# Optimization experiments

Measured on AMD Instinct MI355X. Metric: run time of the kernel, lower is better.

Reference implementation:

```python
import jax, jax.numpy as jnp
import numpy as np
from jax import lax

B, C, H, W = 8192, 256, 5, 5
G = 8
SE_HID = 64        # max(8, 256 // 4)
GN_EPS = 1e-5
MM_EPS = 1e-8


def group_norm(x, gamma, beta):
    # x: [B, C, H, W]; normalize per (group, H, W)
    b = x.shape[0]
    xg = x.reshape(b, G, C // G, H, W)
    mean = xg.mean(axis=(2, 3, 4), keepdims=True)
    var = xg.var(axis=(2, 3, 4), keepdims=True)
    xg = (xg - mean) * lax.rsqrt(var + GN_EPS)
    xn = xg.reshape(b, C, H, W)
    return xn * gamma[None, :, None, None] + beta[None, :, None, None]


def setup_inputs() -> dict:
    key = jax.random.key(0)
    ks = jax.random.split(key, 10)
    x = jax.random.normal(ks[0], (B, C, H, W), dtype=jnp.float32)
    pair_mask = (jax.random.uniform(ks[1], (B, 1, H, W)) < 0.8).astype(jnp.float32)
    s1 = 1.0 / np.sqrt(C)
    W1 = jax.random.normal(ks[2], (C, C), dtype=jnp.float32) * s1          # 1x1 conv
    W2 = jax.random.normal(ks[3], (C, C, 3, 3), dtype=jnp.float32) * (s1 / 3.0)
    g1 = jnp.ones((C,), jnp.float32); b1 = jnp.zeros((C,), jnp.float32)
    g2 = jnp.ones((C,), jnp.float32); b2 = jnp.zeros((C,), jnp.float32)
    fc1_w = jax.random.normal(ks[4], (SE_HID, C), dtype=jnp.float32) * s1
    fc1_b = jnp.zeros((SE_HID,), jnp.float32)
    fc2_w = jax.random.normal(ks[5], (C, SE_HID), dtype=jnp.float32) / np.sqrt(SE_HID)
    fc2_b = jnp.zeros((C,), jnp.float32)
    return {"x": x, "pair_mask": pair_mask, "W1": W1, "g1": g1, "b1": b1,
            "W2": W2, "g2": g2, "b2": b2,
            "fc1_w": fc1_w, "fc1_b": fc1_b, "fc2_w": fc2_w, "fc2_b": fc2_b}


def reference(x, pair_mask, W1, g1, b1, W2, g2, b2, fc1_w, fc1_b, fc2_w, fc2_b):
    residual = x
    # conv1: 1x1, no bias -> channel mixing
    out = jnp.einsum('bchw,oc->bohw', x, W1)
    out = jax.nn.gelu(group_norm(out, g1, b1), approximate=False)
    # conv2: 3x3, padding=1, no bias
    out = lax.conv_general_dilated(out, W2, window_strides=(1, 1),
                                   padding=((1, 1), (1, 1)),
                                   dimension_numbers=('NCHW', 'OIHW', 'NCHW'))
    out = jax.nn.gelu(group_norm(out, g2, b2), approximate=False)
    out = out + residual
    # masked SE
    denom = jnp.maximum(pair_mask.sum(axis=(-1, -2)), MM_EPS)   # [B,1]
    pooled = (out * pair_mask).sum(axis=(-1, -2)) / denom       # [B,C]
    h = jax.nn.gelu(pooled @ fc1_w.T + fc1_b, approximate=False)
    gate = jax.nn.sigmoid(h @ fc2_w.T + fc2_b)                  # [B,C]
    out = out * gate[:, :, None, None] * pair_mask              # SE mask
    out = out * pair_mask                                       # final mask
    return out, gate
```

## Files before the change

kernel.cpp:

```cpp
#include <hip/hip_runtime.h>
#include <math.h>


typedef short v8s  __attribute__((ext_vector_type(8)));
typedef short v4s  __attribute__((ext_vector_type(4)));
typedef float v16f __attribute__((ext_vector_type(16)));
typedef float v4f  __attribute__((ext_vector_type(4)));

#define NTHREADS 512
#define NB 2
#define CPB 560
#define YROWS 49
#define YSB (YROWS*CPB)

#define Y_BYTES  (NB*YSB)
#define GB_OFF   (Y_BYTES)
#define MASK_OFF (GB_OFF + 4096)
#define POOL_OFF (MASK_OFF + 256)
#define H_OFF    (POOL_OFF + 2048)
#define GATE_OFF (H_OFF + 512)
#define INVD_OFF (GATE_OFF + 2048)
#define SMEM_BYTES (INVD_OFF + 64)

__device__ __forceinline__ unsigned short f2bf(float f){
  unsigned u = __float_as_uint(f);
  u = u + 0x7fffu + ((u >> 16) & 1u);
  return (unsigned short)(u >> 16);
}
__device__ __forceinline__ float gelu_f(float v){
  float z  = fabsf(v) * 0.70710678118654752f;
  float t  = __builtin_amdgcn_rcpf(fmaf(0.3275911f, z, 1.0f));
  float e  = __builtin_amdgcn_exp2f(-z*z*1.4426950408889634f);
  float p  = fmaf(1.061405429f, t, -1.453152027f);
  p = fmaf(p, t, 1.421413741f);
  p = fmaf(p, t, -0.284496736f);
  p = fmaf(p, t, 0.254829592f);
  float er = fmaf(-p*t, e, 1.0f);
  er = __builtin_copysignf(er, v);
  return 0.5f*v*(1.0f + er);
}

__device__ __forceinline__ void v16store(char* dst, const v16f &v){
  #pragma unroll
  for (int q=0;q<4;++q){
    v4f t; t[0]=v[4*q]; t[1]=v[4*q+1]; t[2]=v[4*q+2]; t[3]=v[4*q+3];
    *(v4f*)(dst + q*1024) = t;
  }
}
__device__ __forceinline__ void v16addload(const char* src, v16f &v){
  #pragma unroll
  for (int q=0;q<4;++q){
    v4f t = *(const v4f*)(src + q*1024);
    v[4*q]+=t[0]; v[4*q+1]+=t[1]; v[4*q+2]+=t[2]; v[4*q+3]+=t[3];
  }
}

__global__ void prep_kernel(const float* __restrict__ W1, const float* __restrict__ W2,
                            const float* __restrict__ fc1w, const float* __restrict__ fc2w,
                            unsigned short* __restrict__ w1p, unsigned short* __restrict__ w2p,
                            float* __restrict__ fc1t, float* __restrict__ fc2t)
{
  int t = blockIdx.x*blockDim.x + threadIdx.x;
  int stride = gridDim.x*blockDim.x;
  for (int i=t; i<16*256*16; i+=stride){
    int s=i>>12, o=(i>>4)&255, kk=i&15;
    w1p[i] = f2bf(W1[o*256 + s*16 + kk]);
  }
  for (int i=t; i<144*256*16; i+=stride){
    int s=i>>12, o=(i>>4)&255, kk=i&15;
    int kh = (s >= 72) ? 1 : 0;
    int r  = s - kh*72;
    int tap = r>>3, u = r&7;
    int ck = kh*128 + u*16 + kk;
    w2p[i] = f2bf(W2[o*2304 + ck*9 + tap]);
  }
  for (int i=t; i<256*64; i+=stride){ int c=i>>6, h=i&63; fc1t[i]=fc1w[h*256+c]; }
  for (int i=t; i<64*256; i+=stride){ int k=i>>8, c=i&255; fc2t[i]=fc2w[c*64+k]; }
}

__global__ __launch_bounds__(NTHREADS, 4) void lrb_main(
    const float* __restrict__ xg, const float* __restrict__ maskg,
    const float* __restrict__ g1, const float* __restrict__ b1,
    const float* __restrict__ g2, const float* __restrict__ b2,
    const unsigned short* __restrict__ w1p, const unsigned short* __restrict__ w2p,
    const float* __restrict__ fc1t, const float* __restrict__ fc1b,
    const float* __restrict__ fc2t, const float* __restrict__ fc2b,
    float* __restrict__ outg, float* __restrict__ gateg)
{
  extern __shared__ char smem[];
  float* OUTF = (float*)smem;
  float* GB   = (float*)(smem + GB_OFF);
  float* MS   = (float*)(smem + MASK_OFF);
  float* POOL = (float*)(smem + POOL_OFF);
  float* HS   = (float*)(smem + H_OFF);
  float* GT   = (float*)(smem + GATE_OFF);
  float* INVD = (float*)(smem + INVD_OFF);

  const int tid  = threadIdx.x;
  const int lane = tid & 63;
  const int wid  = tid >> 6;
  const int mp   = wid >> 1;
  const int kh   = wid & 1;
  const int p    = lane & 31;
  const int half = lane >> 5;
  const int hx   = half << 4;
  const bool pv  = (p < 25);
  const int b0   = blockIdx.x * NB;

  {
    int4 z4; z4.x=z4.y=z4.z=z4.w=0;
    for (int i = tid; i < NB*24*35; i += NTHREADS){
      int nbb = i / 840;
      int rem = i - nbb*840;
      int rr  = 25 + rem/35, cc = rem - (rem/35)*35;
      *(int4*)(smem + nbb*YSB + rr*CPB + cc*16) = z4;
    }
    if (tid < 256){
      GB[tid]=g1[tid]; GB[256+tid]=b1[tid]; GB[512+tid]=g2[tid]; GB[768+tid]=b2[tid];
    }
    if (tid >= 256 && tid < 256 + NB*32){
      int t2 = tid - 256;
      int nbb = t2>>5, pp = t2&31;
      MS[t2] = (pp < 25) ? maskg[(size_t)(b0+nbb)*25 + pp] : 0.f;
    }
  }

  const int pr = p/5, ps = p - 5*(p/5);
  const int pbase = pv ? (7*pr + ps) : 0;
  const int bcol  = hx + kh*256;
  const char* w1c = (const char*)w1p;
  const char* w2c = (const char*)w2p;
  const int aoff1 = (wid*32 + p)*32 + hx;
  const char* w2k = w2c + kh*589824 + mp*2048 + p*32 + hx;
  const char* Yb1[2] = { smem + p*CPB + hx, smem + YSB + p*CPB + hx };

  v8s A1[3], B1[3][2];
  #pragma unroll
  for (int s0=0; s0<3; ++s0) A1[s0] = *(const v8s*)(w1c + s0*8192 + aoff1);

  for (int i = tid; i < NB*25*32; i += NTHREADS){
    int nbb = i / 800;
    int rem = i - nbb*800;
    int pp  = rem >> 5;
    int c8  = rem & 31;
    const float* src = xg + ((size_t)(b0+nbb)*256 + c8*8)*25 + pp;
    v8s pk;
    #pragma unroll
    for (int k=0;k<8;++k) pk[k] = (short)f2bf(src[k*25]);
    *(v8s*)(smem + nbb*YSB + pp*CPB + c8*16) = pk;
  }
  __syncthreads();

  if (tid < NB){
    float s=0.f;
    #pragma unroll
    for (int pp=0;pp<25;++pp) s += MS[tid*32+pp];
    INVD[tid] = __builtin_amdgcn_rcpf(fmaxf(s, 1e-8f));
  }

  v16f acc1_0, acc1_1;
  #pragma unroll
  for (int j=0;j<16;++j){ acc1_0[j]=0.f; acc1_1[j]=0.f; }
  #pragma unroll
  for (int s0=0; s0<3; ++s0){
    B1[s0][0] = *(const v8s*)(Yb1[0] + s0*32);
    B1[s0][1] = *(const v8s*)(Yb1[1] + s0*32);
  }
  #pragma unroll
  for (int s=0; s<16; ++s){
    __builtin_amdgcn_s_setprio(1);
    acc1_0 = __builtin_amdgcn_mfma_f32_32x32x16_bf16(A1[s%3], B1[s%3][0], acc1_0, 0,0,0);
    acc1_1 = __builtin_amdgcn_mfma_f32_32x32x16_bf16(A1[s%3], B1[s%3][1], acc1_1, 0,0,0);
    __builtin_amdgcn_s_setprio(0);
    if (s+3 < 16){
      A1[s%3] = *(const v8s*)(w1c + (s+3)*8192 + aoff1);
      B1[s%3][0] = *(const v8s*)(Yb1[0] + (s+3)*32);
      B1[s%3][1] = *(const v8s*)(Yb1[1] + (s+3)*32);
    }
  }

  {
    float s0a=0.f,q0a=0.f,s1a=0.f,q1a=0.f;
    #pragma unroll
    for (int j=0;j<16;++j){
      float v0 = acc1_0[j], v1 = acc1_1[j];
      s0a+=v0; q0a+=v0*v0; s1a+=v1; q1a+=v1*v1;
    }
    #pragma unroll
    for (int off=1; off<64; off<<=1){
      s0a += __shfl_xor(s0a, off, 64); q0a += __shfl_xor(q0a, off, 64);
      s1a += __shfl_xor(s1a, off, 64); q1a += __shfl_xor(q1a, off, 64);
    }
    __syncthreads();

    const int grow = pbase + 8;
    float mu0 = s0a*(1.f/800.f), mu1 = s1a*(1.f/800.f);
    float rstd0 = rsqrtf(q0a*(1.f/800.f) - mu0*mu0 + 1e-5f);
    float rstd1 = rsqrtf(q1a*(1.f/800.f) - mu1*mu1 + 1e-5f);
    if (pv){
      #pragma unroll
      for (int nt=0; nt<2; ++nt){
        float mu = nt ? mu1 : mu0, rstd = nt ? rstd1 : rstd0;
        char* dst = smem + nt*YSB + grow*CPB + wid*64 + half*8;
        #pragma unroll
        for (int q=0;q<4;++q){
          v4s pk;
          #pragma unroll
          for (int i2=0;i2<4;++i2){
            int ch = wid*32 + q*8 + half*4 + i2;
            float v = nt ? acc1_1[4*q+i2] : acc1_0[4*q+i2];
            float f = (v-mu)*rstd*GB[ch]+GB[256+ch];
            pk[i2] = (short)f2bf(gelu_f(f));
          }
          *(v4s*)(dst + q*16) = pk;
        }
      }
    }
  }
  {
    int4 z4; z4.x=z4.y=z4.z=z4.w=0;
    for (int i = tid; i < NB*12*35; i += NTHREADS){
      int nbb = i / 420;
      int rem = i - nbb*420;
      int rr  = rem/35, cc = rem - (rem/35)*35;
      int row = rr < 8 ? rr : (rr < 10 ? rr + 5 : rr + 10);
      *(int4*)(smem + nbb*YSB + row*CPB + cc*16) = z4;
    }
  }

  v8s A2[3][2], B2[3][2];
  #pragma unroll
  for (int s0=0; s0<3; ++s0){
    A2[s0][0] = *(const v8s*)(w2k + s0*8192);
    A2[s0][1] = *(const v8s*)(w2k + s0*8192 + 1024);
  }
  __syncthreads();

  v16f acc2_00, acc2_01, acc2_10, acc2_11;
  #pragma unroll
  for (int j=0;j<16;++j){ acc2_00[j]=0.f; acc2_01[j]=0.f; acc2_10[j]=0.f; acc2_11[j]=0.f; }

  {
    int bq = pv ? pbase*CPB : 41*CPB;
    const int bd = pv ? 7*CPB : 0;
    int tb = 0;

    #pragma unroll
    for (int s0=0; s0<3; ++s0){
      B2[s0][0] = *(const v8s*)(smem + bq + bcol + s0*32);
      B2[s0][1] = *(const v8s*)(smem + YSB + bq + bcol + s0*32);
    }

#define C2_STEP(S, PF) do { \
    __builtin_amdgcn_s_setprio(1); \
    acc2_00 = __builtin_amdgcn_mfma_f32_32x32x16_bf16(A2[(S)%3][0], B2[(S)%3][0], acc2_00, 0,0,0); \
    acc2_01 = __builtin_amdgcn_mfma_f32_32x32x16_bf16(A2[(S)%3][0], B2[(S)%3][1], acc2_01, 0,0,0); \
    acc2_10 = __builtin_amdgcn_mfma_f32_32x32x16_bf16(A2[(S)%3][1], B2[(S)%3][0], acc2_10, 0,0,0); \
    acc2_11 = __builtin_amdgcn_mfma_f32_32x32x16_bf16(A2[(S)%3][1], B2[(S)%3][1], acc2_11, 0,0,0); \
    __builtin_amdgcn_s_setprio(0); \
    if (PF) { \
      const char* ap_ = w2k + tb + ((S)+3)*8192; \
      A2[(S)%3][0] = *(const v8s*)(ap_); \
      A2[(S)%3][1] = *(const v8s*)(ap_ + 1024); \
      const int ro_ = (((S)+3) < 24) ? (((S)+3)>>3)*CPB : 7*CPB; \
      const int co_ = (((S)+3)&7)*32; \
      B2[(S)%3][0] = *(const v8s*)(smem + bq + ro_ + bcol + co_); \
      B2[(S)%3][1] = *(const v8s*)(smem + YSB + bq + ro_ + bcol + co_); \
    } \
  } while(0)

    #pragma unroll 1
    for (int tr=0; tr<2; ++tr){
      #pragma unroll
      for (int s=0; s<24; ++s) C2_STEP(s, 1);
      tb += 196608;
      bq += bd;
    }
    #pragma unroll
    for (int s=0; s<21; ++s) C2_STEP(s, 1);
    #pragma unroll
    for (int s=21; s<24; ++s) C2_STEP(s, 0);
#undef C2_STEP
  }
  __syncthreads();

  {
    char* EXw = smem + (kh^1)*16384 + mp*4096 + (lane<<4);
    const char* EXr = smem + kh*16384 + mp*4096 + (lane<<4);
    if (kh==0) v16store(EXw, acc2_01); else v16store(EXw, acc2_00);
    __syncthreads();
    if (kh==0) v16addload(EXr, acc2_00); else v16addload(EXr, acc2_01);
    __syncthreads();
    if (kh==0) v16store(EXw, acc2_11); else v16store(EXw, acc2_10);
    __syncthreads();
    if (kh==0) v16addload(EXr, acc2_10); else v16addload(EXr, acc2_11);
  }
  v16f F0 = (kh==0) ? acc2_00 : acc2_01;
  v16f F1 = (kh==0) ? acc2_10 : acc2_11;

  {
    float s0a=0.f,q0a=0.f,s1a=0.f,q1a=0.f;
    #pragma unroll
    for (int j=0;j<16;++j){
      float v0=F0[j], v1=F1[j];
      s0a+=v0; q0a+=v0*v0; s1a+=v1; q1a+=v1*v1;
    }
    #pragma unroll
    for (int off=1; off<64; off<<=1){
      s0a += __shfl_xor(s0a, off, 64); q0a += __shfl_xor(q0a, off, 64);
      s1a += __shfl_xor(s1a, off, 64); q1a += __shfl_xor(q1a, off, 64);
    }
    __syncthreads();

    float mu0 = s0a*(1.f/800.f), mu1 = s1a*(1.f/800.f);
    float rstd0 = rsqrtf(q0a*(1.f/800.f) - mu0*mu0 + 1e-5f);
    float rstd1 = rsqrtf(q1a*(1.f/800.f) - mu1*mu1 + 1e-5f);
    const float* xr = xg + ((size_t)(b0+kh)*256 + mp*64)*25 + p;
    if (pv){
      #pragma unroll
      for (int j=0;j<16;++j){
        int crow = (j&3) + 8*(j>>2) + 4*half;
        {
          int ch = mp*64 + crow;
          float f = (F0[j]-mu0)*rstd0*GB[512+ch]+GB[768+ch];
          f = gelu_f(f) + xr[crow*25];
          OUTF[kh*6400 + ch*25 + p] = f;
        }
        {
          int ch = mp*64 + 32 + crow;
          float f = (F1[j]-mu1)*rstd1*GB[512+ch]+GB[768+ch];
          f = gelu_f(f) + xr[(32+crow)*25];
          OUTF[kh*6400 + ch*25 + p] = f;
        }
      }
    }
  }
  __syncthreads();

  {
    int nbb = tid >> 8, ch = tid & 255;
    const float* of = OUTF + nbb*6400 + ch*25;
    const float* ms = MS + nbb*32;
    float dot = 0.f;
    #pragma unroll
    for (int pp=0; pp<25; ++pp) dot = fmaf(of[pp], ms[pp], dot);
    POOL[nbb*256 + ch] = dot;
  }
  __syncthreads();

  {
    int nbb  = tid >> 8;
    int hid  = (tid >> 2) & 63;
    int part = tid & 3;
    const float* pl = POOL + nbb*256 + part*64;
    const float* wp = fc1t + part*64*64 + hid;
    float dot = 0.f;
    #pragma unroll 8
    for (int c=0;c<64;++c) dot += wp[c*64]*pl[c];
    dot += __shfl_xor(dot, 1, 64);
    dot += __shfl_xor(dot, 2, 64);
    if (part == 0)
      HS[nbb*64+hid] = gelu_f(fmaf(INVD[nbb], dot, fc1b[hid]));
  }
  __syncthreads();
  {
    int ch = tid & 255, nbb = tid >> 8;
    const float* hp = HS + nbb*64;
    float dot = 0.f;
    #pragma unroll 8
    for (int k=0;k<64;++k) dot += fc2t[k*256+ch]*hp[k];
    dot += fc2b[ch];
    float gv = __builtin_amdgcn_rcpf(1.0f + __builtin_amdgcn_exp2f(-dot*1.4426950408889634f));
    GT[nbb*256+ch] = gv;
    gateg[(size_t)(b0+nbb)*256+ch] = gv;
  }
  __syncthreads();

  for (int i = tid; i < NB*1600; i += NTHREADS){
    int nbb = i / 1600;
    int r4  = i - nbb*1600;
    int e0  = r4*4;
    v4f o4 = *(const v4f*)(OUTF + nbb*6400 + e0);
    #pragma unroll
    for (int k=0;k<4;++k){
      int e = e0+k;
      int ch = e/25;
      int pp = e - ch*25;
      o4[k] = o4[k] * GT[nbb*256+ch] * MS[nbb*32+pp];
    }
    *(v4f*)(outg + (size_t)(b0+nbb)*6400 + e0) = o4;
  }
}

extern "C" void kernel_launch(void* const* d_in, const int* in_sizes, int n_in,
                              void* d_out, int out_size, void* d_ws, size_t ws_size,
                              hipStream_t stream)
{
  const float* xg   = (const float*)d_in[0];
  const float* pm   = (const float*)d_in[1];
  const float* W1   = (const float*)d_in[2];
  const float* g1   = (const float*)d_in[3];
  const float* b1   = (const float*)d_in[4];
  const float* W2   = (const float*)d_in[5];
  const float* g2   = (const float*)d_in[6];
  const float* b2   = (const float*)d_in[7];
  const float* fc1w = (const float*)d_in[8];
  const float* fc1b = (const float*)d_in[9];
  const float* fc2w = (const float*)d_in[10];
  const float* fc2b = (const float*)d_in[11];

  float* outg  = (float*)d_out;
  float* gateg = outg + (size_t)8192*256*25;

  unsigned short* w1p = (unsigned short*)d_ws;
  unsigned short* w2p = w1p + 16*256*16;
  float* fc1t = (float*)(w2p + 144*256*16);
  float* fc2t = fc1t + 256*64;

  prep_kernel<<<dim3(512), dim3(256), 0, stream>>>(W1, W2, fc1w, fc2w, w1p, w2p, fc1t, fc2t);

  hipFuncSetAttribute(reinterpret_cast<const void*>(lrb_main),
                      hipFuncAttributeMaxDynamicSharedMemorySize, (int)SMEM_BYTES);
  lrb_main<<<dim3(4096), dim3(NTHREADS), SMEM_BYTES, stream>>>(
      xg, pm, g1, b1, g2, b2, w1p, w2p, fc1t, fc1b, fc2t, fc2b, outg, gateg);
}
```

Measured before the change: 540.6 us.

## Restructure 3x3 conv as per-wave 144-step MFMA loop with bf16 staging for occupancy

```diff
diff --git a/kernel.cpp b/kernel.cpp
--- a/kernel.cpp
+++ b/kernel.cpp
@@ -9,8 +9,8 @@
 
 #define NTHREADS 512
 #define NB 2
-#define CPB 560
-#define YROWS 49
+#define CPB 528
+#define YROWS 26
 #define YSB (YROWS*CPB)
 
 #define Y_BYTES  (NB*YSB)
@@ -26,6 +26,9 @@
   unsigned u = __float_as_uint(f);
   u = u + 0x7fffu + ((u >> 16) & 1u);
   return (unsigned short)(u >> 16);
+}
+__device__ __forceinline__ float bf2f(unsigned short u){
+  return __uint_as_float(((unsigned)u) << 16);
 }
 __device__ __forceinline__ float gelu_f(float v){
   float z  = fabsf(v) * 0.70710678118654752f;
@@ -40,21 +43,6 @@
   return 0.5f*v*(1.0f + er);
 }
 
-__device__ __forceinline__ void v16store(char* dst, const v16f &v){
-  #pragma unroll
-  for (int q=0;q<4;++q){
-    v4f t; t[0]=v[4*q]; t[1]=v[4*q+1]; t[2]=v[4*q+2]; t[3]=v[4*q+3];
-    *(v4f*)(dst + q*1024) = t;
-  }
-}
-__device__ __forceinline__ void v16addload(const char* src, v16f &v){
-  #pragma unroll
-  for (int q=0;q<4;++q){
-    v4f t = *(const v4f*)(src + q*1024);
-    v[4*q]+=t[0]; v[4*q+1]+=t[1]; v[4*q+2]+=t[2]; v[4*q+3]+=t[3];
-  }
-}
-
 __global__ void prep_kernel(const float* __restrict__ W1, const float* __restrict__ W2,
                             const float* __restrict__ fc1w, const float* __restrict__ fc2w,
                             unsigned short* __restrict__ w1p, unsigned short* __restrict__ w2p,
@@ -68,17 +56,14 @@
   }
   for (int i=t; i<144*256*16; i+=stride){
     int s=i>>12, o=(i>>4)&255, kk=i&15;
-    int kh = (s >= 72) ? 1 : 0;
-    int r  = s - kh*72;
-    int tap = r>>3, u = r&7;
-    int ck = kh*128 + u*16 + kk;
-    w2p[i] = f2bf(W2[o*2304 + ck*9 + tap]);
+    int tap=s>>4, u=s&15;
+    w2p[i] = f2bf(W2[o*2304 + (u*16+kk)*9 + tap]);
   }
   for (int i=t; i<256*64; i+=stride){ int c=i>>6, h=i&63; fc1t[i]=fc1w[h*256+c]; }
   for (int i=t; i<64*256; i+=stride){ int k=i>>8, c=i&255; fc2t[i]=fc2w[c*64+k]; }
 }
 
-__global__ __launch_bounds__(NTHREADS, 4) void lrb_main(
+__global__ __launch_bounds__(NTHREADS, 6) void lrb_main(
     const float* __restrict__ xg, const float* __restrict__ maskg,
     const float* __restrict__ g1, const float* __restrict__ b1,
     const float* __restrict__ g2, const float* __restrict__ b2,
@@ -88,7 +73,7 @@
     float* __restrict__ outg, float* __restrict__ gateg)
 {
   extern __shared__ char smem[];
-  float* OUTF = (float*)smem;
+  unsigned short* OUTFu = (unsigned short*)smem;
   float* GB   = (float*)(smem + GB_OFF);
   float* MS   = (float*)(smem + MASK_OFF);
   float* POOL = (float*)(smem + POOL_OFF);
@@ -99,8 +84,6 @@
   const int tid  = threadIdx.x;
   const int lane = tid & 63;
   const int wid  = tid >> 6;
-  const int mp   = wid >> 1;
-  const int kh   = wid & 1;
   const int p    = lane & 31;
   const int half = lane >> 5;
   const int hx   = half << 4;
@@ -109,34 +92,40 @@
 
   {
     int4 z4; z4.x=z4.y=z4.z=z4.w=0;
-    for (int i = tid; i < NB*24*35; i += NTHREADS){
-      int nbb = i / 840;
-      int rem = i - nbb*840;
-      int rr  = 25 + rem/35, cc = rem - (rem/35)*35;
-      *(int4*)(smem + nbb*YSB + rr*CPB + cc*16) = z4;
-    }
-    if (tid < 256){
-      GB[tid]=g1[tid]; GB[256+tid]=b1[tid]; GB[512+tid]=g2[tid]; GB[768+tid]=b2[tid];
-    }
-    if (tid >= 256 && tid < 256 + NB*32){
-      int t2 = tid - 256;
+    if (tid < 2*33){
+      int nt = tid/33, cc = tid - nt*33;
+      *(int4*)(smem + nt*YSB + 25*CPB + cc*16) = z4;
+    }
+    if (tid >= 64 && tid < 320){
+      int c = tid - 64;
+      GB[c]=g1[c]; GB[256+c]=b1[c]; GB[512+c]=g2[c]; GB[768+c]=b2[c];
+    }
+    if (tid >= 320 && tid < 320 + NB*32){
+      int t2 = tid - 320;
       int nbb = t2>>5, pp = t2&31;
       MS[t2] = (pp < 25) ? maskg[(size_t)(b0+nbb)*25 + pp] : 0.f;
     }
   }
 
   const int pr = p/5, ps = p - 5*(p/5);
-  const int pbase = pv ? (7*pr + ps) : 0;
-  const int bcol  = hx + kh*256;
-  const char* w1c = (const char*)w1p;
-  const char* w2c = (const char*)w2p;
-  const int aoff1 = (wid*32 + p)*32 + hx;
-  const char* w2k = w2c + kh*589824 + mp*2048 + p*32 + hx;
-  const char* Yb1[2] = { smem + p*CPB + hx, smem + YSB + p*CPB + hx };
-
-  v8s A1[3], B1[3][2];
-  #pragma unroll
-  for (int s0=0; s0<3; ++s0) A1[s0] = *(const v8s*)(w1c + s0*8192 + aoff1);
+  const int aoff = (wid*32 + p)*32 + hx;
+  const char* w1a = (const char*)w1p + aoff;
+  const char* w2a = (const char*)w2p + aoff;
+  const int prow1 = pv ? p : 25;
+  const char* b1base[2] = { smem + prow1*CPB + hx, smem + YSB + prow1*CPB + hx };
+
+  int roA[9];
+  #pragma unroll
+  for (int t=0; t<9; ++t){
+    int dr = t/3, ds = t - 3*(t/3);
+    bool v = pv && (pr+dr >= 1) && (pr+dr <= 5) && (ps+ds >= 1) && (ps+ds <= 5);
+    int row = v ? (p + (dr-1)*5 + (ds-1)) : 25;
+    roA[t] = row*CPB + hx;
+  }
+
+  v8s A1[2], B1[2][2];
+  A1[0] = *(const v8s*)(w1a);
+  A1[1] = *(const v8s*)(w1a + 8192);
 
   for (int i = tid; i < NB*25*32; i += NTHREADS){
     int nbb = i / 800;
@@ -162,22 +151,26 @@
   #pragma unroll
   for (int j=0;j<16;++j){ acc1_0[j]=0.f; acc1_1[j]=0.f; }
   #pragma unroll
-  for (int s0=0; s0<3; ++s0){
-    B1[s0][0] = *(const v8s*)(Yb1[0] + s0*32);
-    B1[s0][1] = *(const v8s*)(Yb1[1] + s0*32);
+  for (int s0=0; s0<2; ++s0){
+    B1[s0][0] = *(const v8s*)(b1base[0] + s0*32);
+    B1[s0][1] = *(const v8s*)(b1base[1] + s0*32);
   }
   #pragma unroll
   for (int s=0; s<16; ++s){
     __builtin_amdgcn_s_setprio(1);
-    acc1_0 = __builtin_amdgcn_mfma_f32_32x32x16_bf16(A1[s%3], B1[s%3][0], acc1_0, 0,0,0);
-    acc1_1 = __builtin_amdgcn_mfma_f32_32x32x16_bf16(A1[s%3], B1[s%3][1], acc1_1, 0,0,0);
+    acc1_0 = __builtin_amdgcn_mfma_f32_32x32x16_bf16(A1[s&1], B1[s&1][0], acc1_0, 0,0,0);
+    acc1_1 = __builtin_amdgcn_mfma_f32_32x32x16_bf16(A1[s&1], B1[s&1][1], acc1_1, 0,0,0);
     __builtin_amdgcn_s_setprio(0);
-    if (s+3 < 16){
-      A1[s%3] = *(const v8s*)(w1c + (s+3)*8192 + aoff1);
-      B1[s%3][0] = *(const v8s*)(Yb1[0] + (s+3)*32);
-      B1[s%3][1] = *(const v8s*)(Yb1[1] + (s+3)*32);
-    }
-  }
+    if (s+2 < 16){
+      A1[s&1] = *(const v8s*)(w1a + (s+2)*8192);
+      B1[s&1][0] = *(const v8s*)(b1base[0] + (s+2)*32);
+      B1[s&1][1] = *(const v8s*)(b1base[1] + (s+2)*32);
+    }
+  }
+
+  v8s A2[2], B2[2][2];
+  A2[0] = *(const v8s*)(w2a);
+  A2[1] = *(const v8s*)(w2a + 8192);
 
   {
     float s0a=0.f,q0a=0.f,s1a=0.f,q1a=0.f;
@@ -193,7 +186,6 @@
     }
     __syncthreads();
 
-    const int grow = pbase + 8;
     float mu0 = s0a*(1.f/800.f), mu1 = s1a*(1.f/800.f);
     float rstd0 = rsqrtf(q0a*(1.f/800.f) - mu0*mu0 + 1e-5f);
     float rstd1 = rsqrtf(q1a*(1.f/800.f) - mu1*mu1 + 1e-5f);
@@ -201,7 +193,7 @@
       #pragma unroll
       for (int nt=0; nt<2; ++nt){
         float mu = nt ? mu1 : mu0, rstd = nt ? rstd1 : rstd0;
-        char* dst = smem + nt*YSB + grow*CPB + wid*64 + half*8;
+        char* dst = smem + nt*YSB + p*CPB + wid*64 + half*8;
         #pragma unroll
         for (int q=0;q<4;++q){
           v4s pk;
@@ -217,92 +209,38 @@
       }
     }
   }
-  {
-    int4 z4; z4.x=z4.y=z4.z=z4.w=0;
-    for (int i = tid; i < NB*12*35; i += NTHREADS){
-      int nbb = i / 420;
-      int rem = i - nbb*420;
-      int rr  = rem/35, cc = rem - (rem/35)*35;
-      int row = rr < 8 ? rr : (rr < 10 ? rr + 5 : rr + 10);
-      *(int4*)(smem + nbb*YSB + row*CPB + cc*16) = z4;
-    }
-  }
-
-  v8s A2[3][2], B2[3][2];
-  #pragma unroll
-  for (int s0=0; s0<3; ++s0){
-    A2[s0][0] = *(const v8s*)(w2k + s0*8192);
-    A2[s0][1] = *(const v8s*)(w2k + s0*8192 + 1024);
-  }
-  __syncthreads();
-
-  v16f acc2_00, acc2_01, acc2_10, acc2_11;
-  #pragma unroll
-  for (int j=0;j<16;++j){ acc2_00[j]=0.f; acc2_01[j]=0.f; acc2_10[j]=0.f; acc2_11[j]=0.f; }
-
-  {
-    int bq = pv ? pbase*CPB : 41*CPB;
-    const int bd = pv ? 7*CPB : 0;
-    int tb = 0;
-
-    #pragma unroll
-    for (int s0=0; s0<3; ++s0){
-      B2[s0][0] = *(const v8s*)(smem + bq + bcol + s0*32);
-      B2[s0][1] = *(const v8s*)(smem + YSB + bq + bcol + s0*32);
-    }
-
-#define C2_STEP(S, PF) do { \
-    __builtin_amdgcn_s_setprio(1); \
-    acc2_00 = __builtin_amdgcn_mfma_f32_32x32x16_bf16(A2[(S)%3][0], B2[(S)%3][0], acc2_00, 0,0,0); \
-    acc2_01 = __builtin_amdgcn_mfma_f32_32x32x16_bf16(A2[(S)%3][0], B2[(S)%3][1], acc2_01, 0,0,0); \
-    acc2_10 = __builtin_amdgcn_mfma_f32_32x32x16_bf16(A2[(S)%3][1], B2[(S)%3][0], acc2_10, 0,0,0); \
-    acc2_11 = __builtin_amdgcn_mfma_f32_32x32x16_bf16(A2[(S)%3][1], B2[(S)%3][1], acc2_11, 0,0,0); \
-    __builtin_amdgcn_s_setprio(0); \
-    if (PF) { \
-      const char* ap_ = w2k + tb + ((S)+3)*8192; \
-      A2[(S)%3][0] = *(const v8s*)(ap_); \
-      A2[(S)%3][1] = *(const v8s*)(ap_ + 1024); \
-      const int ro_ = (((S)+3) < 24) ? (((S)+3)>>3)*CPB : 7*CPB; \
-      const int co_ = (((S)+3)&7)*32; \
-      B2[(S)%3][0] = *(const v8s*)(smem + bq + ro_ + bcol + co_); \
-      B2[(S)%3][1] = *(const v8s*)(smem + YSB + bq + ro_ + bcol + co_); \
-    } \
-  } while(0)
-
-    #pragma unroll 1
-    for (int tr=0; tr<2; ++tr){
-      #pragma unroll
-      for (int s=0; s<24; ++s) C2_STEP(s, 1);
-      tb += 196608;
-      bq += bd;
-    }
-    #pragma unroll
-    for (int s=0; s<21; ++s) C2_STEP(s, 1);
-    #pragma unroll
-    for (int s=21; s<24; ++s) C2_STEP(s, 0);
-#undef C2_STEP
-  }
-  __syncthreads();
-
-  {
-    char* EXw = smem + (kh^1)*16384 + mp*4096 + (lane<<4);
-    const char* EXr = smem + kh*16384 + mp*4096 + (lane<<4);
-    if (kh==0) v16store(EXw, acc2_01); else v16store(EXw, acc2_00);
-    __syncthreads();
-    if (kh==0) v16addload(EXr, acc2_00); else v16addload(EXr, acc2_01);
-    __syncthreads();
-    if (kh==0) v16store(EXw, acc2_11); else v16store(EXw, acc2_10);
-    __syncthreads();
-    if (kh==0) v16addload(EXr, acc2_10); else v16addload(EXr, acc2_11);
-  }
-  v16f F0 = (kh==0) ? acc2_00 : acc2_01;
-  v16f F1 = (kh==0) ? acc2_10 : acc2_11;
+  __syncthreads();
+
+  v16f acc2_0, acc2_1;
+  #pragma unroll
+  for (int j=0;j<16;++j){ acc2_0[j]=0.f; acc2_1[j]=0.f; }
+
+  #pragma unroll
+  for (int s0=0; s0<2; ++s0){
+    B2[s0][0] = *(const v8s*)(smem + roA[0] + s0*32);
+    B2[s0][1] = *(const v8s*)(smem + YSB + roA[0] + s0*32);
+  }
+  #pragma unroll
+  for (int s=0; s<144; ++s){
+    __builtin_amdgcn_s_setprio(1);
+    acc2_0 = __builtin_amdgcn_mfma_f32_32x32x16_bf16(A2[s&1], B2[s&1][0], acc2_0, 0,0,0);
+    acc2_1 = __builtin_amdgcn_mfma_f32_32x32x16_bf16(A2[s&1], B2[s&1][1], acc2_1, 0,0,0);
+    __builtin_amdgcn_s_setprio(0);
+    if (s+2 < 144){
+      int s2 = s+2;
+      A2[s&1] = *(const v8s*)(w2a + s2*8192);
+      int ro = roA[s2>>4];
+      int co = (s2&15)*32;
+      B2[s&1][0] = *(const v8s*)(smem + ro + co);
+      B2[s&1][1] = *(const v8s*)(smem + YSB + ro + co);
+    }
+  }
 
   {
     float s0a=0.f,q0a=0.f,s1a=0.f,q1a=0.f;
     #pragma unroll
     for (int j=0;j<16;++j){
-      float v0=F0[j], v1=F1[j];
+      float v0=acc2_0[j], v1=acc2_1[j];
       s0a+=v0; q0a+=v0*v0; s1a+=v1; q1a+=v1*v1;
     }
     #pragma unroll
@@ -315,23 +253,19 @@
     float mu0 = s0a*(1.f/800.f), mu1 = s1a*(1.f/800.f);
     float rstd0 = rsqrtf(q0a*(1.f/800.f) - mu0*mu0 + 1e-5f);
     float rstd1 = rsqrtf(q1a*(1.f/800.f) - mu1*mu1 + 1e-5f);
-    const float* xr = xg + ((size_t)(b0+kh)*256 + mp*64)*25 + p;
     if (pv){
-      #pragma unroll
+      const float* xr0 = xg + ((size_t)(b0+0)*256 + wid*32)*25 + p;
+      const float* xr1 = xg + ((size_t)(b0+1)*256 + wid*32)*25 + p;
+      #pragma unroll 4
       for (int j=0;j<16;++j){
         int crow = (j&3) + 8*(j>>2) + 4*half;
-        {
-          int ch = mp*64 + crow;
-          float f = (F0[j]-mu0)*rstd0*GB[512+ch]+GB[768+ch];
-          f = gelu_f(f) + xr[crow*25];
-          OUTF[kh*6400 + ch*25 + p] = f;
-        }
-        {
-          int ch = mp*64 + 32 + crow;
-          float f = (F1[j]-mu1)*rstd1*GB[512+ch]+GB[768+ch];
-          f = gelu_f(f) + xr[(32+crow)*25];
-          OUTF[kh*6400 + ch*25 + p] = f;
-        }
+        int ch   = wid*32 + crow;
+        float f0 = (acc2_0[j]-mu0)*rstd0*GB[512+ch]+GB[768+ch];
+        f0 = gelu_f(f0) + xr0[crow*25];
+        OUTFu[ch*25 + p] = f2bf(f0);
+        float f1 = (acc2_1[j]-mu1)*rstd1*GB[512+ch]+GB[768+ch];
+        f1 = gelu_f(f1) + xr1[crow*25];
+        OUTFu[6400 + ch*25 + p] = f2bf(f1);
       }
     }
   }
@@ -339,11 +273,11 @@
 
   {
     int nbb = tid >> 8, ch = tid & 255;
-    const float* of = OUTF + nbb*6400 + ch*25;
+    const unsigned short* of = OUTFu + nbb*6400 + ch*25;
     const float* ms = MS + nbb*32;
     float dot = 0.f;
     #pragma unroll
-    for (int pp=0; pp<25; ++pp) dot = fmaf(of[pp], ms[pp], dot);
+    for (int pp=0; pp<25; ++pp) dot = fmaf(bf2f(of[pp]), ms[pp], dot);
     POOL[nbb*256 + ch] = dot;
   }
   __syncthreads();
@@ -376,19 +310,25 @@
   }
   __syncthreads();
 
-  for (int i = tid; i < NB*1600; i += NTHREADS){
-    int nbb = i / 1600;
-    int r4  = i - nbb*1600;
-    int e0  = r4*4;
-    v4f o4 = *(const v4f*)(OUTF + nbb*6400 + e0);
-    #pragma unroll
-    for (int k=0;k<4;++k){
+  for (int i = tid; i < NB*800; i += NTHREADS){
+    int nbb = (i >= 800);
+    int r   = i - nbb*800;
+    int e0  = r*8;
+    v8s pk = *(const v8s*)(OUTFu + nbb*6400 + e0);
+    float o[8];
+    #pragma unroll
+    for (int k=0;k<8;++k){
       int e = e0+k;
       int ch = e/25;
       int pp = e - ch*25;
-      o4[k] = o4[k] * GT[nbb*256+ch] * MS[nbb*32+pp];
-    }
-    *(v4f*)(outg + (size_t)(b0+nbb)*6400 + e0) = o4;
+      o[k] = bf2f((unsigned short)pk[k]) * GT[nbb*256+ch] * MS[nbb*32+pp];
+    }
+    float* dst = outg + (size_t)(b0+nbb)*6400 + e0;
+    v4f a, b;
+    a[0]=o[0]; a[1]=o[1]; a[2]=o[2]; a[3]=o[3];
+    b[0]=o[4]; b[1]=o[5]; b[2]=o[6]; b[3]=o[7];
+    *(v4f*)(dst)   = a;
+    *(v4f*)(dst+4) = b;
   }
 }
 
```

New measurement: 548.5 us. Within noise of the previous version (+1.5%).
